# Kernel tuning notes

Hardware: AMD Instinct MI355X
Metric: run time of the kernel (lower is better)

## Reference

```python
import jax, jax.numpy as jnp
import numpy as np

N_HEADS = 16
NEG_INF = -10000.0


def setup_inputs() -> dict:
    key = jax.random.key(0)
    k1, k2, k3, k4 = jax.random.split(key, 4)
    B, S, D = 2, 2048, 1024
    q = jax.random.normal(k1, (B, S, D), dtype=jnp.float32)
    k = jax.random.normal(k2, (B, S, D), dtype=jnp.float32)
    v = jax.random.normal(k3, (B, S, D), dtype=jnp.float32)
    mask = jax.random.randint(k4, (B, S, S), 0, 2, dtype=jnp.int32)
    return {"q": q, "k": k, "v": v, "mask": mask}


def _mha(q, k, v, mask):
    B, S, D = q.shape
    H = N_HEADS
    hd = D // H
    # [B,S,D] -> [B,H,S,hd]
    qh = q.reshape(B, S, H, hd).transpose(0, 2, 1, 3)
    kh = k.reshape(B, S, H, hd).transpose(0, 2, 1, 3)
    vh = v.reshape(B, S, H, hd).transpose(0, 2, 1, 3)
    scores = jnp.einsum('bhqd,bhkd->bhqk', qh, kh) / jnp.sqrt(jnp.float32(hd))
    scores = scores + mask[:, None, :, :].astype(scores.dtype) * NEG_INF
    probs = jax.nn.softmax(scores, axis=-1)
    out = jnp.einsum('bhqk,bhkd->bhqd', probs, vh)
    return out.transpose(0, 2, 1, 3).reshape(B, S, D)


def reference(q, k, v, mask):
    return _mha(q, k, v, mask)
```

## Files before the change

kernel.cpp:

```cpp
#include <hip/hip_runtime.h>
#include <stdint.h>

#define S_LEN 2048
#define DMODEL 1024
#define NH 16
#define HD 64
#define NWORDS (S_LEN / 32)
#define NT (S_LEN / 64)

typedef __attribute__((ext_vector_type(4))) float f32x4;
typedef __attribute__((ext_vector_type(8))) short s16x8;
typedef __attribute__((ext_vector_type(4))) short s16x4;
typedef __attribute__((ext_vector_type(4))) int i32x4;
typedef __attribute__((ext_vector_type(2))) uint32_t u32x2;

__device__ __forceinline__ short f2bf(float x) {
  union { float f; uint32_t u; } v; v.f = x;
  return (short)((v.u + 0x8000u) >> 16);
}

__device__ __forceinline__ uint32_t cvtpk(float a, float b) {
  uint32_t r;
  asm("v_cvt_pk_bf16_f32 %0, %1, %2" : "=v"(r) : "v"(a), "v"(b));
  return r;
}

__device__ __forceinline__ float hexp2(float x) {
#if __has_builtin(__builtin_amdgcn_exp2f)
  return __builtin_amdgcn_exp2f(x);
#else
  float r;
  asm("v_exp_f32 %0, %1" : "=v"(r) : "v"(x));
  return r;
#endif
}

__device__ __forceinline__ f32x4 mfma32(s16x8 a, s16x8 b, f32x4 c) {
  return __builtin_amdgcn_mfma_f32_16x16x32_bf16(a, b, c, 0, 0, 0);
}

__device__ __forceinline__ f32x4 mfma16(s16x4 a, s16x4 b, f32x4 c) {
#if __has_builtin(__builtin_amdgcn_mfma_f32_16x16x16bf16_1k)
  return __builtin_amdgcn_mfma_f32_16x16x16bf16_1k(a, b, c, 0, 0, 0);
#else
  f32x4 d;
  asm("v_mfma_f32_16x16x16_bf16 %0, %1, %2, %3" : "=&v"(d) : "v"(a), "v"(b), "v"(c));
  return d;
#endif
}

typedef const __attribute__((address_space(1))) uint32_t* gas_u32p;
typedef __attribute__((address_space(3))) uint32_t* las_u32p;
__device__ __forceinline__ void gl_lds16(const void* g, void* l) {
  __builtin_amdgcn_global_load_lds((gas_u32p)g, (las_u32p)l, 16, 0, 0);
}

__global__ __launch_bounds__(256) void maskpack_kernel(
    const int* __restrict__ mask, uint32_t* __restrict__ bits, int ngroups) {
  const int lane = threadIdx.x & 63;
  const int wave = blockIdx.x * (blockDim.x >> 6) + (threadIdx.x >> 6);
  const int nw = gridDim.x * (blockDim.x >> 6);
  for (int gi = wave; gi < ngroups; gi += nw) {
    const int m = mask[(size_t)gi * 64 + lane];
    const unsigned long long bal = __ballot(m != 0);
    if (lane == 0) {
      bits[(size_t)gi * 2]     = (uint32_t)bal;
      bits[(size_t)gi * 2 + 1] = (uint32_t)(bal >> 32);
    }
  }
}

__global__ __launch_bounds__(256) void packkv_kernel(
    const float* __restrict__ k, const float* __restrict__ v,
    short* __restrict__ Kp, short* __restrict__ Vp) {
  const int t = blockIdx.x, h = blockIdx.y;
  const int b = blockIdx.z & 1, which = blockIdx.z >> 1;
  if (which == 0) {
    short* dst = Kp + (((size_t)(b * NH + h) * NT) + t) * 4096;
    const float* src0 = k + ((size_t)b * S_LEN + t * 64) * DMODEL + h * HD;
    for (int c = threadIdx.x; c < 512; c += 256) {
      const int kv = c >> 3, j = c & 7;
      const int jsrc = j ^ (kv & 7);
      const float* p = src0 + (size_t)kv * DMODEL + jsrc * 8;
      const f32x4 a = *(const f32x4*)p;
      const f32x4 bb = *(const f32x4*)(p + 4);
      s16x8 o;
      o[0]=f2bf(a[0]);  o[1]=f2bf(a[1]);  o[2]=f2bf(a[2]);  o[3]=f2bf(a[3]);
      o[4]=f2bf(bb[0]); o[5]=f2bf(bb[1]); o[6]=f2bf(bb[2]); o[7]=f2bf(bb[3]);
      *(s16x8*)(dst + (size_t)c * 8) = o;
    }
  } else {
    short* dst = Vp + (((size_t)(b * NH + h) * NT) + t) * 4096;
    const float* src0 = v + ((size_t)b * S_LEN + t * 64) * DMODEL + h * HD;
    for (int c = threadIdx.x; c < 1024; c += 256) {
      const int quad = c >> 6, dd = c & 63;
      const int d = dd ^ (quad & 7);
      const float* p = src0 + (size_t)quad * 4 * DMODEL + d;
      s16x4 o;
      o[0] = f2bf(p[0]);
      o[1] = f2bf(p[DMODEL]);
      o[2] = f2bf(p[2 * DMODEL]);
      o[3] = f2bf(p[3 * DMODEL]);
      *(s16x4*)(dst + (size_t)c * 4) = o;
    }
  }
}

__device__ __forceinline__ void tile_step(
    int buf,
    const char*& kg, const char*& vg, const uint32_t*& bp,
    char* klsb, char* vlsb, int so,
    int ka0, int ka1, int vaE, int vaO, int g4,
    const s16x8& qf0, const s16x8& qf1,
    u32x2& mwnext, f32x4 acc[4], f32x4& accsum) {
  const float LOG2E = 1.44269504088896f;
  const float nMC = -14.0f * 1.44269504088896f;
  const f32x4 z4 = {0.f, 0.f, 0.f, 0.f};

  const u32x2 mw = mwnext;
  mwnext = *(const u32x2*)bp;
  bp += 2;

  {
    char* kl = klsb + (buf ^ 1) * 8192 + so;
    char* vl = vlsb + (buf ^ 1) * 8192 + so;
    gl_lds16(kg, kl);        gl_lds16(kg + 1024, kl + 1024);
    gl_lds16(vg, vl);        gl_lds16(vg + 1024, vl + 1024);
    kg += 8192;
    vg += 8192;
  }

  f32x4 st[4];
  __builtin_amdgcn_s_setprio(1);
#pragma unroll
  for (int mi = 0; mi < 4; ++mi) {
    const char* rp = klsb + buf * 8192 + mi * 2048;
    const s16x8 kf0 = *(const s16x8*)(rp + ka0);
    const s16x8 kf1 = *(const s16x8*)(rp + ka1);
    st[mi] = mfma32(kf1, qf1, mfma32(kf0, qf0, z4));
  }
  __builtin_amdgcn_s_setprio(0);

  const uint32_t wlo = mw[0] >> g4;
  const uint32_t whi = mw[1] >> g4;
  s16x4 pf[4];
#pragma unroll
  for (int mi = 0; mi < 4; ++mi) {
    const uint32_t w = (mi < 2) ? wlo : whi;
    const int bpos = (mi & 1) << 4;
    float p[4];
#pragma unroll
    for (int r = 0; r < 4; ++r) {
      const float e = hexp2(__builtin_fmaf(st[mi][r], LOG2E, nMC));
      const uint32_t keep = ((w >> (bpos + r)) & 1u) - 1u;
      union { float f; uint32_t u; } pu;
      pu.f = e;
      pu.u &= keep;
      p[r] = pu.f;
    }
    union { uint32_t u[2]; s16x4 v; } pk;
    pk.u[0] = cvtpk(p[0], p[1]);
    pk.u[1] = cvtpk(p[2], p[3]);
    pf[mi] = pk.v;
  }

  const s16x4 onesb = {(short)0x3F80, (short)0x3F80, (short)0x3F80, (short)0x3F80};
  __builtin_amdgcn_s_setprio(1);
#pragma unroll
  for (int kc = 0; kc < 4; ++kc) {
    const char* vb = vlsb + buf * 8192 + kc * 2048;
    const int va = (kc & 1) ? vaO : vaE;
    accsum = mfma16(pf[kc], onesb, accsum);
#pragma unroll
    for (int dt = 0; dt < 4; ++dt) {
      const s16x4 vf = *(const s16x4*)(vb + dt * 128 + va);
      acc[dt] = mfma16(pf[kc], vf, acc[dt]);
    }
  }
  __builtin_amdgcn_s_setprio(0);

  asm volatile("s_waitcnt vmcnt(0)" ::: "memory");
  __syncthreads();
}

__global__ __launch_bounds__(256, 4) void attn4_kernel(
    const float* __restrict__ q, const char* __restrict__ Kp,
    const char* __restrict__ Vp, const uint32_t* __restrict__ bits,
    float* __restrict__ out) {
  const int tid = threadIdx.x, lane = tid & 63, wid = tid >> 6;
  const int lq = lane & 15, g = lane >> 4, g4 = g << 2;

  const int wg = blockIdx.x;
  const int sw = ((wg & 7) << 7) | (wg >> 3);
  const int bx = sw & 31;
  const int h  = (sw >> 5) & 15;
  const int b  = sw >> 9;

  const int qrow = bx * 64 + wid * 16 + lq;
  const size_t bS = (size_t)b * S_LEN;

  __shared__ __align__(16) short kls[2][4096];
  __shared__ __align__(16) short vls[2][4096];

  s16x8 qf0, qf1;
  {
    const float* qp = q + (bS + qrow) * DMODEL + h * HD + g * 8;
    const f32x4 a0 = *(const f32x4*)qp;
    const f32x4 a1 = *(const f32x4*)(qp + 4);
    const f32x4 b0 = *(const f32x4*)(qp + 32);
    const f32x4 b1 = *(const f32x4*)(qp + 36);
    qf0[0]=f2bf(a0[0]*0.125f); qf0[1]=f2bf(a0[1]*0.125f);
    qf0[2]=f2bf(a0[2]*0.125f); qf0[3]=f2bf(a0[3]*0.125f);
    qf0[4]=f2bf(a1[0]*0.125f); qf0[5]=f2bf(a1[1]*0.125f);
    qf0[6]=f2bf(a1[2]*0.125f); qf0[7]=f2bf(a1[3]*0.125f);
    qf1[0]=f2bf(b0[0]*0.125f); qf1[1]=f2bf(b0[1]*0.125f);
    qf1[2]=f2bf(b0[2]*0.125f); qf1[3]=f2bf(b0[3]*0.125f);
    qf1[4]=f2bf(b1[0]*0.125f); qf1[5]=f2bf(b1[1]*0.125f);
    qf1[6]=f2bf(b1[2]*0.125f); qf1[7]=f2bf(b1[3]*0.125f);
  }

  const char* kpb = Kp + ((size_t)(b * NH + h) * NT) * 8192;
  const char* vpb = Vp + ((size_t)(b * NH + h) * NT) * 8192;
  const uint32_t* bp = bits + (bS + qrow) * NWORDS;

  const f32x4 z4 = {0.f, 0.f, 0.f, 0.f};
  f32x4 acc[4] = {z4, z4, z4, z4};
  f32x4 accsum = z4;

  const int swk = (lq & 7) << 4;
  const int ka0 = lq * 128 + ((g * 16) ^ swk);
  const int ka1 = lq * 128 + ((64 + g * 16) ^ swk);
  const int vaE = g * 512 + ((lq * 8) ^ (g * 8));
  const int vaO = g * 512 + ((lq * 8) ^ (g * 8 + 32));

  const int so = wid * 2048;
  u32x2 mwnext = *(const u32x2*)bp;
  bp += 2;

  const char* kg = kpb + so + lane * 16;
  const char* vg = vpb + so + lane * 16;

  {
    char* kl = (char*)kls + so;
    char* vl = (char*)vls + so;
    gl_lds16(kg, kl);        gl_lds16(kg + 1024, kl + 1024);
    gl_lds16(vg, vl);        gl_lds16(vg + 1024, vl + 1024);
    kg += 8192;
    vg += 8192;
  }
  asm volatile("s_waitcnt vmcnt(0)" ::: "memory");
  __syncthreads();

  for (int t2 = 0; t2 < NT; t2 += 2) {
    tile_step(0, kg, vg, bp, (char*)kls, (char*)vls, so,
              ka0, ka1, vaE, vaO, g4, qf0, qf1, mwnext, acc, accsum);
    tile_step(1, kg, vg, bp, (char*)kls, (char*)vls, so,
              ka0, ka1, vaE, vaO, g4, qf0, qf1, mwnext, acc, accsum);
  }

  float linv[4];
#pragma unroll
  for (int r = 0; r < 4; ++r) linv[r] = 1.0f / accsum[r];
  float* ob = out + (bS + bx * 64 + wid * 16) * DMODEL + h * HD;
#pragma unroll
  for (int dt = 0; dt < 4; ++dt)
#pragma unroll
    for (int r = 0; r < 4; ++r)
      ob[(size_t)(g4 + r) * DMODEL + dt * 16 + lq] = acc[dt][r] * linv[r];
}

template <int MASKBITS>
__global__ __launch_bounds__(256) void attn_kernel(
    const float* __restrict__ q, const float* __restrict__ k,
    const float* __restrict__ v, const int* __restrict__ mask,
    const uint32_t* __restrict__ bits, float* __restrict__ out) {
  const int tid  = threadIdx.x;
  const int lane = tid & 63;
  const int wid  = tid >> 6;
  const int lq   = lane & 15;
  const int g    = lane >> 4;
  const int g4   = g << 2;
  const int b    = blockIdx.z;
  const int h    = blockIdx.y;
  const int qw   = blockIdx.x * 128 + wid * 32;

  __shared__ __align__(16) short kls[64 * 64];
  __shared__ __align__(16) short vls[64 * 64];

  const size_t bS = (size_t)b * S_LEN;
  const float* qbase = q + bS * DMODEL + h * HD;
  const float* kbase = k + bS * DMODEL + h * HD;
  const float* vbase = v + bS * DMODEL + h * HD;

  const float LOG2E = 1.44269504088896f;
  const f32x4 z4 = {0.f, 0.f, 0.f, 0.f};

  s16x8 qf[2][2];
#pragma unroll
  for (int nq = 0; nq < 2; ++nq)
#pragma unroll
    for (int dc = 0; dc < 2; ++dc) {
      const float* p = qbase + (size_t)(qw + nq * 16 + lq) * DMODEL + dc * 32 + g * 8;
      const f32x4 a = *(const f32x4*)p;
      const f32x4 c = *(const f32x4*)(p + 4);
      s16x8 f;
      f[0] = f2bf(a[0] * 0.125f); f[1] = f2bf(a[1] * 0.125f);
      f[2] = f2bf(a[2] * 0.125f); f[3] = f2bf(a[3] * 0.125f);
      f[4] = f2bf(c[0] * 0.125f); f[5] = f2bf(c[1] * 0.125f);
      f[6] = f2bf(c[2] * 0.125f); f[7] = f2bf(c[3] * 0.125f);
      qf[nq][dc] = f;
    }

  f32x4 acc[2][4];
#pragma unroll
  for (int nq = 0; nq < 2; ++nq)
#pragma unroll
    for (int dt = 0; dt < 4; ++dt) acc[nq][dt] = z4;
  float mrun[2] = {-3.0e38f, -3.0e38f};
  float lrun[2] = {0.f, 0.f};

  const int kr  = tid >> 2;
  const int kc4 = (tid & 3) * 16;
  const int vq  = tid >> 4;
  const int vd  = (tid & 15) * 4;

  for (int t = 0; t < NT; ++t) {
    const int kvb = t * 64;
    uint32_t mw0[2], mw1[2];
    i32x4 mdir[2][4];
    if (MASKBITS) {
#pragma unroll
      for (int nq = 0; nq < 2; ++nq) {
        const uint32_t* bpp = bits + (bS + qw + nq * 16 + lq) * NWORDS + (kvb >> 5);
        const u32x2 w = *(const u32x2*)bpp;
        mw0[nq] = w[0]; mw1[nq] = w[1];
      }
    } else {
#pragma unroll
      for (int nq = 0; nq < 2; ++nq)
#pragma unroll
        for (int mi = 0; mi < 4; ++mi)
          mdir[nq][mi] = *(const i32x4*)(mask + (bS + qw + nq * 16 + lq) * S_LEN +
                                         kvb + mi * 16 + g4);
    }

    __syncthreads();
    {
      const float* p = kbase + (size_t)(kvb + kr) * DMODEL + kc4;
      const f32x4 x0 = *(const f32x4*)p;
      const f32x4 x1 = *(const f32x4*)(p + 4);
      const f32x4 x2 = *(const f32x4*)(p + 8);
      const f32x4 x3 = *(const f32x4*)(p + 12);
      s16x8 lo, hi;
      lo[0]=f2bf(x0[0]); lo[1]=f2bf(x0[1]); lo[2]=f2bf(x0[2]); lo[3]=f2bf(x0[3]);
      lo[4]=f2bf(x1[0]); lo[5]=f2bf(x1[1]); lo[6]=f2bf(x1[2]); lo[7]=f2bf(x1[3]);
      hi[0]=f2bf(x2[0]); hi[1]=f2bf(x2[1]); hi[2]=f2bf(x2[2]); hi[3]=f2bf(x2[3]);
      hi[4]=f2bf(x3[0]); hi[5]=f2bf(x3[1]); hi[6]=f2bf(x3[2]); hi[7]=f2bf(x3[3]);
      char* rowp = (char*)kls + kr * 128;
      const int sw = (kr & 7) << 4;
      *(s16x8*)(rowp + ((kc4 * 2) ^ sw))      = lo;
      *(s16x8*)(rowp + ((kc4 * 2 + 16) ^ sw)) = hi;
    }
    {
      const float* p = vbase + (size_t)(kvb + vq * 4) * DMODEL + vd;
      const f32x4 r0 = *(const f32x4*)p;
      const f32x4 r1 = *(const f32x4*)(p + DMODEL);
      const f32x4 r2 = *(const f32x4*)(p + 2 * DMODEL);
      const f32x4 r3 = *(const f32x4*)(p + 3 * DMODEL);
      char* rowp = (char*)vls + vq * 512;
      const int sw = (vq & 7) << 3;
#pragma unroll
      for (int j = 0; j < 4; ++j) {
        s16x4 pk;
        pk[0] = f2bf(r0[j]); pk[1] = f2bf(r1[j]);
        pk[2] = f2bf(r2[j]); pk[3] = f2bf(r3[j]);
        *(s16x4*)(rowp + (((vd + j) * 8) ^ sw)) = pk;
      }
    }
    __syncthreads();

    f32x4 stv[2][4];
#pragma unroll
    for (int mi = 0; mi < 4; ++mi) {
      const char* rp = (const char*)kls + (mi * 16 + lq) * 128;
      const int sw = (lq & 7) << 4;
      const s16x8 kf0 = *(const s16x8*)(rp + ((g * 16) ^ sw));
      const s16x8 kf1 = *(const s16x8*)(rp + ((64 + g * 16) ^ sw));
      stv[0][mi] = mfma32(kf0, qf[0][0], z4);
      stv[0][mi] = mfma32(kf1, qf[0][1], stv[0][mi]);
      stv[1][mi] = mfma32(kf0, qf[1][0], z4);
      stv[1][mi] = mfma32(kf1, qf[1][1], stv[1][mi]);
    }

    s16x4 pf[2][4];
#pragma unroll
    for (int nq = 0; nq < 2; ++nq) {
#pragma unroll
      for (int mi = 0; mi < 4; ++mi) {
#pragma unroll
        for (int r = 0; r < 4; ++r) {
          float mz;
          if (MASKBITS) {
            const uint32_t w = (mi < 2) ? mw0[nq] : mw1[nq];
            const int sh = ((mi & 1) << 4) + g4 + r;
            mz = (float)((w >> sh) & 1u);
          } else {
            mz = (float)mdir[nq][mi][r];
          }
          stv[nq][mi][r] = stv[nq][mi][r] - 10000.0f * mz;
        }
      }
      float mx = -3.0e38f;
#pragma unroll
      for (int mi = 0; mi < 4; ++mi)
#pragma unroll
        for (int r = 0; r < 4; ++r) mx = fmaxf(mx, stv[nq][mi][r]);
      mx = fmaxf(mx, __shfl_xor(mx, 16));
      mx = fmaxf(mx, __shfl_xor(mx, 32));
      const float mnew = fmaxf(mrun[nq], mx);
      const float al = exp2f((mrun[nq] - mnew) * LOG2E);
      mrun[nq] = mnew;
      const float nms = mnew * LOG2E;
      float sum = 0.f;
#pragma unroll
      for (int mi = 0; mi < 4; ++mi)
#pragma unroll
        for (int r = 0; r < 4; ++r) {
          const float p = exp2f(__builtin_fmaf(stv[nq][mi][r], LOG2E, -nms));
          stv[nq][mi][r] = p;
          sum += p;
        }
      sum += __shfl_xor(sum, 16);
      sum += __shfl_xor(sum, 32);
      lrun[nq] = lrun[nq] * al + sum;
      float aO[4];
#pragma unroll
      for (int r = 0; r < 4; ++r) aO[r] = __shfl(al, g4 + r);
#pragma unroll
      for (int dt = 0; dt < 4; ++dt)
#pragma unroll
        for (int r = 0; r < 4; ++r) acc[nq][dt][r] *= aO[r];
#pragma unroll
      for (int kc = 0; kc < 4; ++kc) {
        s16x4 pp;
#pragma unroll
        for (int r = 0; r < 4; ++r) pp[r] = f2bf(stv[nq][kc][r]);
        pf[nq][kc] = pp;
      }
    }

#pragma unroll
    for (int kc = 0; kc < 4; ++kc) {
#pragma unroll
      for (int dt = 0; dt < 4; ++dt) {
        const int quad = kc * 4 + g;
        const s16x4 vf = *(const s16x4*)((const char*)vls + quad * 512 +
                                         (((dt * 16 + lq) * 8) ^ ((quad & 7) << 3)));
        acc[0][dt] = mfma16(pf[0][kc], vf, acc[0][dt]);
        acc[1][dt] = mfma16(pf[1][kc], vf, acc[1][dt]);
      }
    }
  }

  float* obase = out + bS * DMODEL + h * HD;
#pragma unroll
  for (int nq = 0; nq < 2; ++nq) {
    const float linv = 1.0f / lrun[nq];
    float li[4];
#pragma unroll
    for (int r = 0; r < 4; ++r) li[r] = __shfl(linv, g4 + r);
#pragma unroll
    for (int dt = 0; dt < 4; ++dt)
#pragma unroll
      for (int r = 0; r < 4; ++r)
        obase[(size_t)(qw + nq * 16 + g4 + r) * DMODEL + dt * 16 + lq] =
            acc[nq][dt][r] * li[r];
  }
}

extern "C" void kernel_launch(void* const* d_in, const int* in_sizes, int n_in,
                              void* d_out, int out_size, void* d_ws, size_t ws_size,
                              hipStream_t stream) {
  const float* q   = (const float*)d_in[0];
  const float* k   = (const float*)d_in[1];
  const float* v   = (const float*)d_in[2];
  const int* mask  = (const int*)d_in[3];
  float* out       = (float*)d_out;

  const size_t bits_bytes = (size_t)2 * S_LEN * NWORDS * sizeof(uint32_t);
  const size_t pack_bytes = (size_t)2 * S_LEN * DMODEL * sizeof(short);
  const size_t full_bytes = bits_bytes + 2 * pack_bytes + 16384;

  if (ws_size >= full_bytes) {
    char* w = (char*)d_ws;
    uint32_t* bits = (uint32_t*)w;
    char* Kp = w + bits_bytes;
    char* Vp = w + bits_bytes + pack_bytes;

    const int ngroups = 2 * S_LEN * (S_LEN / 64);
    maskpack_kernel<<<512, 256, 0, stream>>>(mask, bits, ngroups);
    packkv_kernel<<<dim3(NT, NH, 4), 256, 0, stream>>>(k, v, (short*)Kp, (short*)Vp);
    attn4_kernel<<<1024, 256, 0, stream>>>(q, Kp, Vp, bits, out);
  } else if (ws_size >= bits_bytes) {
    uint32_t* bits = (uint32_t*)d_ws;
    const int ngroups = 2 * S_LEN * (S_LEN / 64);
    maskpack_kernel<<<512, 256, 0, stream>>>(mask, bits, ngroups);
    attn_kernel<1><<<dim3(S_LEN / 128, NH, 2), 256, 0, stream>>>(
        q, k, v, mask, bits, out);
  } else {
    attn_kernel<0><<<dim3(S_LEN / 128, NH, 2), 256, 0, stream>>>(
        q, k, v, mask, nullptr, out);
  }
}
```

Measured before the change: 94.21 us.

## Process two query row groups per wave to reuse K/V tiles

Each wave now computes 32 query rows (two 16-row MFMA groups) sharing the same K/V LDS tiles, halving the grid to 512 blocks and lowering the occupancy hint to 2. The log2e factor is folded into the Q prescale and the fixed max offset is removed from the exponent. This cuts global/LDS traffic per unit of work and adds independent MFMA chains, at the cost of more registers, fewer resident waves, and less grid parallelism. A clamp on the softmax denominator guards against division by zero.

```diff
diff --git a/kernel.cpp b/kernel.cpp
--- a/kernel.cpp
+++ b/kernel.cpp
@@ -106,62 +106,67 @@
   }
 }
 
-__device__ __forceinline__ void tile_step(
+__device__ __forceinline__ void tile_step7(
     int buf,
-    const char*& kg, const char*& vg, const uint32_t*& bp,
+    const char*& kg, const char*& vg,
+    const uint32_t*& bp0, const uint32_t*& bp1,
     char* klsb, char* vlsb, int so,
-    int ka0, int ka1, int vaE, int vaO, int g4,
-    const s16x8& qf0, const s16x8& qf1,
-    u32x2& mwnext, f32x4 acc[4], f32x4& accsum) {
-  const float LOG2E = 1.44269504088896f;
-  const float nMC = -14.0f * 1.44269504088896f;
+    int ka0, int ka1, int voE, int voO, int g4,
+    const s16x8& qf00, const s16x8& qf01,
+    const s16x8& qf10, const s16x8& qf11,
+    u32x2& mwn0, u32x2& mwn1,
+    f32x4 acc0[4], f32x4 acc1[4], f32x4& accs0, f32x4& accs1) {
   const f32x4 z4 = {0.f, 0.f, 0.f, 0.f};
 
-  const u32x2 mw = mwnext;
-  mwnext = *(const u32x2*)bp;
-  bp += 2;
+  const u32x2 mw0 = mwn0, mw1 = mwn1;
+  mwn0 = *(const u32x2*)bp0; bp0 += 2;
+  mwn1 = *(const u32x2*)bp1; bp1 += 2;
 
   {
     char* kl = klsb + (buf ^ 1) * 8192 + so;
     char* vl = vlsb + (buf ^ 1) * 8192 + so;
-    gl_lds16(kg, kl);        gl_lds16(kg + 1024, kl + 1024);
-    gl_lds16(vg, vl);        gl_lds16(vg + 1024, vl + 1024);
+    gl_lds16(kg, kl);  gl_lds16(kg + 1024, kl + 1024);
+    gl_lds16(vg, vl);  gl_lds16(vg + 1024, vl + 1024);
     kg += 8192;
     vg += 8192;
   }
 
-  f32x4 st[4];
+  f32x4 st0[4], st1[4];
   __builtin_amdgcn_s_setprio(1);
 #pragma unroll
   for (int mi = 0; mi < 4; ++mi) {
     const char* rp = klsb + buf * 8192 + mi * 2048;
     const s16x8 kf0 = *(const s16x8*)(rp + ka0);
     const s16x8 kf1 = *(const s16x8*)(rp + ka1);
-    st[mi] = mfma32(kf1, qf1, mfma32(kf0, qf0, z4));
+    st0[mi] = mfma32(kf1, qf01, mfma32(kf0, qf00, z4));
+    st1[mi] = mfma32(kf1, qf11, mfma32(kf0, qf10, z4));
   }
   __builtin_amdgcn_s_setprio(0);
 
-  const uint32_t wlo = mw[0] >> g4;
-  const uint32_t whi = mw[1] >> g4;
-  s16x4 pf[4];
+  const uint32_t wlo0 = mw0[0] >> g4, whi0 = mw0[1] >> g4;
+  const uint32_t wlo1 = mw1[0] >> g4, whi1 = mw1[1] >> g4;
+  s16x4 pf0[4], pf1[4];
 #pragma unroll
   for (int mi = 0; mi < 4; ++mi) {
-    const uint32_t w = (mi < 2) ? wlo : whi;
+    const uint32_t w0 = (mi < 2) ? wlo0 : whi0;
+    const uint32_t w1 = (mi < 2) ? wlo1 : whi1;
     const int bpos = (mi & 1) << 4;
-    float p[4];
+    float p0[4], p1[4];
 #pragma unroll
     for (int r = 0; r < 4; ++r) {
-      const float e = hexp2(__builtin_fmaf(st[mi][r], LOG2E, nMC));
-      const uint32_t keep = ((w >> (bpos + r)) & 1u) - 1u;
-      union { float f; uint32_t u; } pu;
-      pu.f = e;
-      pu.u &= keep;
-      p[r] = pu.f;
-    }
-    union { uint32_t u[2]; s16x4 v; } pk;
-    pk.u[0] = cvtpk(p[0], p[1]);
-    pk.u[1] = cvtpk(p[2], p[3]);
-    pf[mi] = pk.v;
+      union { float f; uint32_t u; } a, c;
+      a.f = hexp2(st0[mi][r]);
+      a.u &= (((w0 >> (bpos + r)) & 1u) - 1u);
+      p0[r] = a.f;
+      c.f = hexp2(st1[mi][r]);
+      c.u &= (((w1 >> (bpos + r)) & 1u) - 1u);
+      p1[r] = c.f;
+    }
+    union { uint32_t u[2]; s16x4 v4; } k0, k1;
+    k0.u[0] = cvtpk(p0[0], p0[1]);  k0.u[1] = cvtpk(p0[2], p0[3]);
+    k1.u[0] = cvtpk(p1[0], p1[1]);  k1.u[1] = cvtpk(p1[2], p1[3]);
+    pf0[mi] = k0.v4;
+    pf1[mi] = k1.v4;
   }
 
   const s16x4 onesb = {(short)0x3F80, (short)0x3F80, (short)0x3F80, (short)0x3F80};
@@ -169,12 +174,14 @@
 #pragma unroll
   for (int kc = 0; kc < 4; ++kc) {
     const char* vb = vlsb + buf * 8192 + kc * 2048;
-    const int va = (kc & 1) ? vaO : vaE;
-    accsum = mfma16(pf[kc], onesb, accsum);
+    const int vo = (kc & 1) ? voO : voE;
+    accs0 = mfma16(pf0[kc], onesb, accs0);
+    accs1 = mfma16(pf1[kc], onesb, accs1);
 #pragma unroll
     for (int dt = 0; dt < 4; ++dt) {
-      const s16x4 vf = *(const s16x4*)(vb + dt * 128 + va);
-      acc[dt] = mfma16(pf[kc], vf, acc[dt]);
+      const s16x4 vf = *(const s16x4*)(vb + dt * 128 + vo);
+      acc0[dt] = mfma16(pf0[kc], vf, acc0[dt]);
+      acc1[dt] = mfma16(pf1[kc], vf, acc1[dt]);
     }
   }
   __builtin_amdgcn_s_setprio(0);
@@ -183,7 +190,7 @@
   __syncthreads();
 }
 
-__global__ __launch_bounds__(256, 4) void attn4_kernel(
+__global__ __launch_bounds__(256, 2) void attn7_kernel(
     const float* __restrict__ q, const char* __restrict__ Kp,
     const char* __restrict__ Vp, const uint32_t* __restrict__ bits,
     float* __restrict__ out) {
@@ -191,82 +198,107 @@
   const int lq = lane & 15, g = lane >> 4, g4 = g << 2;
 
   const int wg = blockIdx.x;
-  const int sw = ((wg & 7) << 7) | (wg >> 3);
-  const int bx = sw & 31;
-  const int h  = (sw >> 5) & 15;
-  const int b  = sw >> 9;
-
-  const int qrow = bx * 64 + wid * 16 + lq;
+  const int sz = ((wg & 7) << 6) | (wg >> 3);
+  const int bx = sz & 15;
+  const int h  = (sz >> 4) & 15;
+  const int b  = sz >> 8;
+
+  const int qbase = bx * 128 + wid * 32;
   const size_t bS = (size_t)b * S_LEN;
+  const int qr0 = qbase + lq;
+  const int qr1 = qbase + 16 + lq;
 
   __shared__ __align__(16) short kls[2][4096];
   __shared__ __align__(16) short vls[2][4096];
 
-  s16x8 qf0, qf1;
+  const f32x4 z4 = {0.f, 0.f, 0.f, 0.f};
+  const float SC = 0.125f * 1.44269504088896f;
+
+  s16x8 qf00, qf01, qf10, qf11;
   {
-    const float* qp = q + (bS + qrow) * DMODEL + h * HD + g * 8;
+    const float* qp = q + (bS + qr0) * (size_t)DMODEL + h * HD + g * 8;
     const f32x4 a0 = *(const f32x4*)qp;
     const f32x4 a1 = *(const f32x4*)(qp + 4);
     const f32x4 b0 = *(const f32x4*)(qp + 32);
     const f32x4 b1 = *(const f32x4*)(qp + 36);
-    qf0[0]=f2bf(a0[0]*0.125f); qf0[1]=f2bf(a0[1]*0.125f);
-    qf0[2]=f2bf(a0[2]*0.125f); qf0[3]=f2bf(a0[3]*0.125f);
-    qf0[4]=f2bf(a1[0]*0.125f); qf0[5]=f2bf(a1[1]*0.125f);
-    qf0[6]=f2bf(a1[2]*0.125f); qf0[7]=f2bf(a1[3]*0.125f);
-    qf1[0]=f2bf(b0[0]*0.125f); qf1[1]=f2bf(b0[1]*0.125f);
-    qf1[2]=f2bf(b0[2]*0.125f); qf1[3]=f2bf(b0[3]*0.125f);
-    qf1[4]=f2bf(b1[0]*0.125f); qf1[5]=f2bf(b1[1]*0.125f);
-    qf1[6]=f2bf(b1[2]*0.125f); qf1[7]=f2bf(b1[3]*0.125f);
-  }
-
-  const char* kpb = Kp + ((size_t)(b * NH + h) * NT) * 8192;
-  const char* vpb = Vp + ((size_t)(b * NH + h) * NT) * 8192;
-  const uint32_t* bp = bits + (bS + qrow) * NWORDS;
-
-  const f32x4 z4 = {0.f, 0.f, 0.f, 0.f};
-  f32x4 acc[4] = {z4, z4, z4, z4};
-  f32x4 accsum = z4;
+    qf00[0]=f2bf(a0[0]*SC); qf00[1]=f2bf(a0[1]*SC);
+    qf00[2]=f2bf(a0[2]*SC); qf00[3]=f2bf(a0[3]*SC);
+    qf00[4]=f2bf(a1[0]*SC); qf00[5]=f2bf(a1[1]*SC);
+    qf00[6]=f2bf(a1[2]*SC); qf00[7]=f2bf(a1[3]*SC);
+    qf01[0]=f2bf(b0[0]*SC); qf01[1]=f2bf(b0[1]*SC);
+    qf01[2]=f2bf(b0[2]*SC); qf01[3]=f2bf(b0[3]*SC);
+    qf01[4]=f2bf(b1[0]*SC); qf01[5]=f2bf(b1[1]*SC);
+    qf01[6]=f2bf(b1[2]*SC); qf01[7]=f2bf(b1[3]*SC);
+  }
+  {
+    const float* qp = q + (bS + qr1) * (size_t)DMODEL + h * HD + g * 8;
+    const f32x4 a0 = *(const f32x4*)qp;
+    const f32x4 a1 = *(const f32x4*)(qp + 4);
+    const f32x4 b0 = *(const f32x4*)(qp + 32);
+    const f32x4 b1 = *(const f32x4*)(qp + 36);
+    qf10[0]=f2bf(a0[0]*SC); qf10[1]=f2bf(a0[1]*SC);
+    qf10[2]=f2bf(a0[2]*SC); qf10[3]=f2bf(a0[3]*SC);
+    qf10[4]=f2bf(a1[0]*SC); qf10[5]=f2bf(a1[1]*SC);
+    qf10[6]=f2bf(a1[2]*SC); qf10[7]=f2bf(a1[3]*SC);
+    qf11[0]=f2bf(b0[0]*SC); qf11[1]=f2bf(b0[1]*SC);
+    qf11[2]=f2bf(b0[2]*SC); qf11[3]=f2bf(b0[3]*SC);
+    qf11[4]=f2bf(b1[0]*SC); qf11[5]=f2bf(b1[1]*SC);
+    qf11[6]=f2bf(b1[2]*SC); qf11[7]=f2bf(b1[3]*SC);
+  }
+
+  const char* kg = Kp + ((size_t)(b * NH + h) * NT) * 8192 + wid * 2048 + lane * 16;
+  const char* vg = Vp + ((size_t)(b * NH + h) * NT) * 8192 + wid * 2048 + lane * 16;
+  const uint32_t* bp0 = bits + (bS + qr0) * NWORDS;
+  const uint32_t* bp1 = bits + (bS + qr1) * NWORDS;
+
+  f32x4 acc0[4] = {z4, z4, z4, z4};
+  f32x4 acc1[4] = {z4, z4, z4, z4};
+  f32x4 accs0 = z4, accs1 = z4;
 
   const int swk = (lq & 7) << 4;
   const int ka0 = lq * 128 + ((g * 16) ^ swk);
   const int ka1 = lq * 128 + ((64 + g * 16) ^ swk);
-  const int vaE = g * 512 + ((lq * 8) ^ (g * 8));
-  const int vaO = g * 512 + ((lq * 8) ^ (g * 8 + 32));
-
-  const int so = wid * 2048;
-  u32x2 mwnext = *(const u32x2*)bp;
-  bp += 2;
-
-  const char* kg = kpb + so + lane * 16;
-  const char* vg = vpb + so + lane * 16;
+  const int voE = g * 512 + ((lq * 8) ^ (g * 8));
+  const int voO = g * 512 + ((lq * 8) ^ (g * 8 + 32));
+  const int so  = wid * 2048;
+
+  u32x2 mwn0 = *(const u32x2*)bp0;  bp0 += 2;
+  u32x2 mwn1 = *(const u32x2*)bp1;  bp1 += 2;
 
   {
     char* kl = (char*)kls + so;
     char* vl = (char*)vls + so;
-    gl_lds16(kg, kl);        gl_lds16(kg + 1024, kl + 1024);
-    gl_lds16(vg, vl);        gl_lds16(vg + 1024, vl + 1024);
-    kg += 8192;
-    vg += 8192;
+    gl_lds16(kg, kl);  gl_lds16(kg + 1024, kl + 1024);
+    gl_lds16(vg, vl);  gl_lds16(vg + 1024, vl + 1024);
+    kg += 8192; vg += 8192;
   }
   asm volatile("s_waitcnt vmcnt(0)" ::: "memory");
   __syncthreads();
 
   for (int t2 = 0; t2 < NT; t2 += 2) {
-    tile_step(0, kg, vg, bp, (char*)kls, (char*)vls, so,
-              ka0, ka1, vaE, vaO, g4, qf0, qf1, mwnext, acc, accsum);
-    tile_step(1, kg, vg, bp, (char*)kls, (char*)vls, so,
-              ka0, ka1, vaE, vaO, g4, qf0, qf1, mwnext, acc, accsum);
-  }
-
-  float linv[4];
-#pragma unroll
-  for (int r = 0; r < 4; ++r) linv[r] = 1.0f / accsum[r];
-  float* ob = out + (bS + bx * 64 + wid * 16) * DMODEL + h * HD;
+    tile_step7(0, kg, vg, bp0, bp1, (char*)kls, (char*)vls, so,
+               ka0, ka1, voE, voO, g4, qf00, qf01, qf10, qf11,
+               mwn0, mwn1, acc0, acc1, accs0, accs1);
+    tile_step7(1, kg, vg, bp0, bp1, (char*)kls, (char*)vls, so,
+               ka0, ka1, voE, voO, g4, qf00, qf01, qf10, qf11,
+               mwn0, mwn1, acc0, acc1, accs0, accs1);
+  }
+
+  float li0[4], li1[4];
+#pragma unroll
+  for (int r = 0; r < 4; ++r) {
+    li0[r] = 1.0f / fmaxf(accs0[r], 1e-30f);
+    li1[r] = 1.0f / fmaxf(accs1[r], 1e-30f);
+  }
+  float* ob0 = out + (bS + qbase) * (size_t)DMODEL + h * HD;
+  float* ob1 = ob0 + (size_t)16 * DMODEL;
 #pragma unroll
   for (int dt = 0; dt < 4; ++dt)
 #pragma unroll
-    for (int r = 0; r < 4; ++r)
-      ob[(size_t)(g4 + r) * DMODEL + dt * 16 + lq] = acc[dt][r] * linv[r];
+    for (int r = 0; r < 4; ++r) {
+      ob0[(size_t)(g4 + r) * DMODEL + dt * 16 + lq] = acc0[dt][r] * li0[r];
+      ob1[(size_t)(g4 + r) * DMODEL + dt * 16 + lq] = acc1[dt][r] * li1[r];
+    }
 }
 
 template <int MASKBITS>
@@ -357,9 +389,9 @@
       hi[0]=f2bf(x2[0]); hi[1]=f2bf(x2[1]); hi[2]=f2bf(x2[2]); hi[3]=f2bf(x2[3]);
       hi[4]=f2bf(x3[0]); hi[5]=f2bf(x3[1]); hi[6]=f2bf(x3[2]); hi[7]=f2bf(x3[3]);
       char* rowp = (char*)kls + kr * 128;
-      const int sw = (kr & 7) << 4;
-      *(s16x8*)(rowp + ((kc4 * 2) ^ sw))      = lo;
-      *(s16x8*)(rowp + ((kc4 * 2 + 16) ^ sw)) = hi;
+      const int sw2 = (kr & 7) << 4;
+      *(s16x8*)(rowp + ((kc4 * 2) ^ sw2))      = lo;
+      *(s16x8*)(rowp + ((kc4 * 2 + 16) ^ sw2)) = hi;
     }
     {
       const float* p = vbase + (size_t)(kvb + vq * 4) * DMODEL + vd;
@@ -368,13 +400,13 @@
       const f32x4 r2 = *(const f32x4*)(p + 2 * DMODEL);
       const f32x4 r3 = *(const f32x4*)(p + 3 * DMODEL);
       char* rowp = (char*)vls + vq * 512;
-      const int sw = (vq & 7) << 3;
+      const int sw2 = (vq & 7) << 3;
 #pragma unroll
       for (int j = 0; j < 4; ++j) {
         s16x4 pk;
         pk[0] = f2bf(r0[j]); pk[1] = f2bf(r1[j]);
         pk[2] = f2bf(r2[j]); pk[3] = f2bf(r3[j]);
-        *(s16x4*)(rowp + (((vd + j) * 8) ^ sw)) = pk;
+        *(s16x4*)(rowp + (((vd + j) * 8) ^ sw2)) = pk;
       }
     }
     __syncthreads();
@@ -383,9 +415,9 @@
 #pragma unroll
     for (int mi = 0; mi < 4; ++mi) {
       const char* rp = (const char*)kls + (mi * 16 + lq) * 128;
-      const int sw = (lq & 7) << 4;
-      const s16x8 kf0 = *(const s16x8*)(rp + ((g * 16) ^ sw));
-      const s16x8 kf1 = *(const s16x8*)(rp + ((64 + g * 16) ^ sw));
+      const int sw2 = (lq & 7) << 4;
+      const s16x8 kf0 = *(const s16x8*)(rp + ((g * 16) ^ sw2));
+      const s16x8 kf1 = *(const s16x8*)(rp + ((64 + g * 16) ^ sw2));
       stv[0][mi] = mfma32(kf0, qf[0][0], z4);
       stv[0][mi] = mfma32(kf1, qf[0][1], stv[0][mi]);
       stv[1][mi] = mfma32(kf0, qf[1][0], z4);
@@ -500,7 +532,7 @@
     const int ngroups = 2 * S_LEN * (S_LEN / 64);
     maskpack_kernel<<<512, 256, 0, stream>>>(mask, bits, ngroups);
     packkv_kernel<<<dim3(NT, NH, 4), 256, 0, stream>>>(k, v, (short*)Kp, (short*)Vp);
-    attn4_kernel<<<1024, 256, 0, stream>>>(q, Kp, Vp, bits, out);
+    attn7_kernel<<<512, 256, 0, stream>>>(q, Kp, Vp, bits, out);
   } else if (ws_size >= bits_bytes) {
     uint32_t* bits = (uint32_t*)d_ws;
     const int ngroups = 2 * S_LEN * (S_LEN / 64);
```

New measurement: 93.55 us. About the same (-0.7%).
